# Kernel tuning notes

Hardware: AMD Instinct MI355X
Metric: run time of the kernel (lower is better)

The kernel has to match this reference:

```python
import jax, jax.numpy as jnp
import numpy as np

NEG = -100.0
M2M, M2I, M2D, I2M, I2I, D2M, D2D = range(7)
LOG_Q = float(np.log(0.25))


def _d_chain(fM, aM2D, aD2D):
    """Sequential delete-state recurrence along motif axis k.
    fD[k] = logaddexp(aM2D[k-1] + fM[k-1], aD2D[k-1] + fD[k-1]), fD[0] = NEG.
    fM: (B, K+1); aM2D, aD2D: (B, K+1). Returns (B, K+1)."""
    B, Kp1 = fM.shape
    K = Kp1 - 1

    def step(fd_prev, inp):
        am, ad, fm = inp  # each (B,)
        fd = jnp.logaddexp(am + fm, ad + fd_prev)
        return fd, fd

    init = jnp.full((B,), NEG, dtype=fM.dtype)
    _, fds = jax.lax.scan(step, init, (aM2D[:, :K].T, aD2D[:, :K].T, fM[:, :K].T))
    return jnp.concatenate([init[:, None], fds.T], axis=1)


def _profile_hmm_loss(a, e, x):
    """pHMM forward algorithm (log-space). a: (B,K+1,7), e: (B,K,4), x: (B,L) int.
    Returns -log P(x) per batch element, shape (B,)."""
    B, Kp1, _ = a.shape
    K = Kp1 - 1

    fM0 = jnp.full((B, Kp1), NEG, dtype=a.dtype).at[:, 0].set(0.0)
    fI0 = jnp.full((B, Kp1), NEG, dtype=a.dtype)
    fD0 = _d_chain(fM0, a[:, :, M2D], a[:, :, D2D])

    def l_step(carry, x_l):
        fM, fI, fD = carry
        # emission for symbol x_l at each match state k: (B, K)
        esel = jnp.take_along_axis(e, x_l[:, None, None].astype(jnp.int32), axis=2)[:, :, 0]
        prev = jnp.logaddexp(
            jnp.logaddexp(a[:, :K, M2M] + fM[:, :K], a[:, :K, I2M] + fI[:, :K]),
            a[:, :K, D2M] + fD[:, :K],
        )
        fM_new = jnp.concatenate([jnp.full((B, 1), NEG, dtype=a.dtype), esel + prev], axis=1)
        fI_new = LOG_Q + jnp.logaddexp(a[:, :, M2I] + fM, a[:, :, I2I] + fI)
        fD_new = _d_chain(fM_new, a[:, :, M2D], a[:, :, D2D])
        return (fM_new, fI_new, fD_new), None

    (fM, fI, fD), _ = jax.lax.scan(l_step, (fM0, fI0, fD0), x.T)

    final = jnp.stack(
        [fM[:, K] + a[:, K, M2M], fI[:, K] + a[:, K, I2M], fD[:, K] + a[:, K, D2M]],
        axis=1,
    )
    return -jax.nn.logsumexp(final, axis=1)


def _kld_loss(mus, logvars):
    return -0.5 * jnp.sum(1.0 + logvars - mus * mus - jnp.exp(logvars), axis=1)


def setup_inputs() -> dict:
    key = jax.random.key(0)
    k1, k2, k3, k4, k5 = jax.random.split(key, 5)
    B, K, L, E = 4096, 64, 128, 16
    batch_input = jax.random.randint(k1, (B, L), 0, 4, dtype=jnp.int32)
    transition_probs = jax.random.normal(k2, (B, K + 1, 7), dtype=jnp.float32)
    emission_probs = jax.random.normal(k3, (B, K, 4), dtype=jnp.float32)
    mus = jax.random.normal(k4, (B, E), dtype=jnp.float32)
    logvars = jax.random.normal(k5, (B, E), dtype=jnp.float32)
    return {
        "batch_input": batch_input,
        "transition_probs": transition_probs,
        "emission_probs": emission_probs,
        "mus": mus,
        "logvars": logvars,
    }


def reference(batch_input, transition_probs, emission_probs, mus, logvars):
    beta = 1.0
    recon = jnp.mean(_profile_hmm_loss(transition_probs, emission_probs, batch_input))
    kld = jnp.mean(_kld_loss(mus, logvars))
    return recon + beta * kld
```

## Files before the change

### kernel.cpp

```cpp
#include <hip/hip_runtime.h>
#include <math.h>


namespace {

constexpr float kLog2e = 1.4426950408889634f;
constexpr float kLn2   = 0.6931471805599453f;

__device__ __forceinline__ float fexp(float x) {
    return __builtin_amdgcn_exp2f(x * kLog2e);
}

__device__ __forceinline__ float rflf(float x) {
    return __builtin_bit_cast(float,
        __builtin_amdgcn_readfirstlane(__builtin_bit_cast(int, x)));
}

template <int CTRL, bool BC>
__device__ __forceinline__ float dppf(float old, float src) {
    int r = __builtin_amdgcn_update_dpp(__builtin_bit_cast(int, old),
                                        __builtin_bit_cast(int, src),
                                        CTRL, 0xF, 0xF, BC);
    return __builtin_bit_cast(float, r);
}

__global__ __launch_bounds__(256) void phmm_vae_kernel(
    const int* __restrict__ xg,
    const float* __restrict__ ag,
    const float* __restrict__ eg,
    const float* __restrict__ mug,
    const float* __restrict__ lvg,
    float* __restrict__ out, int B)
{
    const int tid  = threadIdx.x;
    const int lane = tid & 63;
    const int wv   = tid >> 6;
    const int b    = (blockIdx.x << 2) + wv;

    __shared__ float part[4];
    float contrib = 0.0f;

    if (b < B) {
        const float* ab = ag + (size_t)b * 455;
        const float* eb = eg + (size_t)b * 256;
        const int*   xb = xg + (size_t)b * 128;

        const int j = lane;
        const float a2 = ab[j * 7 + 2];
        const float a6 = ab[j * 7 + 6];
        const float a5 = ab[(j + 1) * 7 + 5];
        const float A1M2M  = fexp(ab[(j + 1) * 7 + 0]);
        const float QA1M2I = 0.25f * fexp(ab[(j + 1) * 7 + 1]);
        const float A1I2M  = fexp(ab[(j + 1) * 7 + 3]);
        const float QA1I2I = 0.25f * fexp(ab[(j + 1) * 7 + 4]);
        const float A0M2M = fexp(ab[0]);
        const float D0f = rflf(0.25f * fexp(ab[4]));
        const float G0f = rflf(0.25f * fexp(ab[3] + ab[1] - ab[0]));

        float4 ev = *reinterpret_cast<const float4*>(eb + j * 4);
        const float E0 = fexp(ev.x), E1 = fexp(ev.y);
        const float E2 = fexp(ev.z), E3 = fexp(ev.w);

        const int xlo = xb[lane];
        const int xhi = xb[64 + lane];
        const unsigned long long b0lo = __ballot(xlo & 1);
        const unsigned long long b1lo = __ballot(xlo & 2);
        const unsigned long long b0hi = __ballot(xhi & 1);
        const unsigned long long b1hi = __ballot(xhi & 2);

        const float a5p = dppf<0x138, false>(0.0f, a5);
        const float dh  = fexp(a6 + a5 - a5p);
        const float wM2D = fexp(a2 + a5);
        const float Cf0 = wM2D * dppf<0x138, false>(0.0f, E0);
        const float Cf1 = wM2D * dppf<0x138, false>(0.0f, E1);
        const float Cf2 = wM2D * dppf<0x138, false>(0.0f, E2);
        const float Cf3 = wM2D * dppf<0x138, false>(0.0f, E3);

        auto bfr = [](float x) -> unsigned {
            unsigned u = __builtin_bit_cast(unsigned, x);
            return (u + 0x8000u) >> 16;
        };
        const int E10 = (int)((bfr(E1) << 16) | bfr(E0));
        const int E32 = (int)((bfr(E3) << 16) | bfr(E2));
        const int C10 = (int)((bfr(Cf1) << 16) | bfr(Cf0));
        const int C32 = (int)((bfr(Cf3) << 16) | bfr(Cf2));

        const float V1 = dh;
        const float V2 = V1 * dppf<0x111, false>(1.0f, V1);
        const float V4 = V2 * dppf<0x112, false>(1.0f, V2);
        const float V8 = V4 * dppf<0x114, false>(1.0f, V4);
        const float V1m = (lane >= 1)  ? V1 : 0.0f;
        const float V2m = (lane >= 2)  ? V2 : 0.0f;
        const float V4m = (lane >= 4)  ? V4 : 0.0f;
        const float V8m = (lane >= 8)  ? V8 : 0.0f;
        float Q = dh;
        Q *= dppf<0x111, false>(1.0f, Q);
        Q *= dppf<0x112, false>(1.0f, Q);
        Q *= dppf<0x114, false>(1.0f, Q);
        Q *= dppf<0x118, false>(1.0f, Q);
        const int   row = lane >> 4;
        const float Q47 = __shfl(Q, 47, 64);
        const float QmA = (row == 1 || row == 3) ? Q : 0.0f;
        const float QmB = (row == 2) ? Q : ((row == 3) ? Q * Q47 : 0.0f);

        float y0 = (lane == 0) ? wM2D : 0.0f;
        y0 = fmaf(V1m, dppf<0x111, true>(0.0f, y0), y0);
        y0 = fmaf(V2m, dppf<0x112, true>(0.0f, y0), y0);
        y0 = fmaf(V4m, dppf<0x114, true>(0.0f, y0), y0);
        y0 = fmaf(V8m, dppf<0x118, true>(0.0f, y0), y0);
        y0 = fmaf(QmA, dppf<0x142, true>(0.0f, y0), y0);
        y0 = fmaf(QmB, dppf<0x143, true>(0.0f, y0), y0);

        auto sel_of = [&](int l) -> int {
            const unsigned long long m0 = (l & 64) ? b0hi : b0lo;
            const unsigned long long m1 = (l & 64) ? b1hi : b1lo;
            const int sh = l & 63;
            unsigned s = (unsigned)((m0 >> sh) & 1ull) |
                         ((unsigned)((m1 >> sh) & 1ull) << 1);
            return (int)(0x00000C0Cu + s * 0x02020000u + 0x01000000u);
        };

        float fM = 0.0f, fI = 0.0f;
        float pl = y0;
        float p0 = A0M2M;
        float LS = 0.0f;

        const int sel0 = sel_of(0);
        float E = __builtin_bit_cast(float,
            __builtin_amdgcn_perm((unsigned)E32, (unsigned)E10, (unsigned)sel0));
        float C = __builtin_bit_cast(float,
            __builtin_amdgcn_perm((unsigned)C32, (unsigned)C10, (unsigned)sel0));

#pragma unroll 8
        for (int l = 0; l < 128; ++l) {
            const int seln = sel_of((l + 1) & 127);
            const float mul_s = (l == 0) ? G0f : D0f;

            float y, pv, En, Cn;
            asm("v_mul_f32 %[fI], %[QI2I], %[fI]\n\t"
                "v_mov_b32 %[pv], %[p0]\n\t"
                "v_perm_b32 %[En], %[e32], %[e10], %[sel]\n\t"
                "v_perm_b32 %[Cn], %[c32], %[c10], %[sel]\n\t"
                "v_mov_b32_dpp %[pv], %[pl] wave_shr:1 row_mask:0xf bank_mask:0xf\n\t"
                "v_fmac_f32 %[fI], %[QM2I], %[fM]\n\t"
                "v_mul_f32 %[p0], %[mul], %[p0]\n\t"
                "v_mul_f32_dpp %[y], %[pv], %[C] wave_shr:1 row_mask:0xf bank_mask:0xf bound_ctrl:0\n\t"
                "v_mul_f32 %[fM], %[E], %[pv]\n\t"
                "s_nop 0\n\t"
                "v_fmac_f32_dpp %[y], %[y], %[V1] row_shr:1 row_mask:0xf bank_mask:0xf bound_ctrl:0\n\t"
                "s_nop 1\n\t"
                "v_fmac_f32_dpp %[y], %[y], %[V2] row_shr:2 row_mask:0xf bank_mask:0xf bound_ctrl:0\n\t"
                "s_nop 1\n\t"
                "v_fmac_f32_dpp %[y], %[y], %[V4] row_shr:4 row_mask:0xf bank_mask:0xf bound_ctrl:0\n\t"
                "s_nop 1\n\t"
                "v_fmac_f32_dpp %[y], %[y], %[V8] row_shr:8 row_mask:0xf bank_mask:0xf bound_ctrl:0\n\t"
                "s_nop 1\n\t"
                "v_fmac_f32_dpp %[y], %[y], %[QmA] row_bcast:15 row_mask:0xf bank_mask:0xf bound_ctrl:0\n\t"
                "s_nop 1\n\t"
                "v_fmac_f32_dpp %[y], %[y], %[QmB] row_bcast:31 row_mask:0xf bank_mask:0xf bound_ctrl:0\n\t"
                "v_fmac_f32 %[y], %[I2M], %[fI]\n\t"
                "v_fmac_f32 %[y], %[M2M], %[fM]"
                : [y] "=&v"(y), [pv] "=&v"(pv), [En] "=&v"(En), [Cn] "=&v"(Cn),
                  [fM] "+v"(fM), [fI] "+v"(fI), [p0] "+v"(p0)
                : [pl] "v"(pl), [E] "v"(E), [C] "v"(C),
                  [e32] "v"(E32), [e10] "v"(E10),
                  [c32] "v"(C32), [c10] "v"(C10),
                  [V1] "v"(V1m), [V2] "v"(V2m), [V4] "v"(V4m), [V8] "v"(V8m),
                  [QmA] "v"(QmA), [QmB] "v"(QmB),
                  [QI2I] "v"(QA1I2I), [QM2I] "v"(QA1M2I),
                  [I2M] "v"(A1I2M), [M2M] "v"(A1M2M),
                  [sel] "s"(seln), [mul] "s"(mul_s));
            pl = y;
            E = En;
            C = Cn;

            if ((l & 15) == 15) {
                float m = fmaxf(fmaxf(fM, fI), pl);
                m = fmaxf(m, dppf<0xB1,  true>(0.0f, m));
                m = fmaxf(m, dppf<0x4E,  true>(0.0f, m));
                m = fmaxf(m, dppf<0x141, true>(0.0f, m));
                m = fmaxf(m, dppf<0x140, true>(0.0f, m));
                m = fmaxf(m, 1e-35f);
                int mb = __builtin_bit_cast(int, m);
                unsigned u0 = (unsigned)__builtin_amdgcn_readlane(mb, 0);
                unsigned u1 = (unsigned)__builtin_amdgcn_readlane(mb, 16);
                unsigned u2 = (unsigned)__builtin_amdgcn_readlane(mb, 32);
                unsigned u3 = (unsigned)__builtin_amdgcn_readlane(mb, 48);
                unsigned ua = u0 > u1 ? u0 : u1;
                unsigned ub = u2 > u3 ? u2 : u3;
                unsigned um = ua > ub ? ua : ub;
                int ee = (int)(um >> 23);
                float r = __builtin_bit_cast(float, (unsigned)(254 - ee) << 23);
                LS += (float)(ee - 127);
                fM *= r; fI *= r; pl *= r; p0 *= r;
            }
        }

        const float Fv = __shfl(pl, 63, 64);
        const float loss = -(__builtin_amdgcn_logf(Fv) + LS) * kLn2;

        float kt = 0.0f;
        if (lane < 16) {
            float mu = mug[(size_t)b * 16 + lane];
            float lv = lvg[(size_t)b * 16 + lane];
            kt = 1.0f + lv - mu * mu - fexp(lv);
        }
        kt += __shfl_xor(kt, 1, 64);
        kt += __shfl_xor(kt, 2, 64);
        kt += __shfl_xor(kt, 4, 64);
        kt += __shfl_xor(kt, 8, 64);
        float kldb = __shfl(-0.5f * kt, 0, 64);

        contrib = (loss + kldb) * (1.0f / 4096.0f);
    }

    if (lane == 63) part[wv] = (b < B) ? contrib : 0.0f;
    __syncthreads();
    if (tid == 0) {
        atomicAdd(out, part[0] + part[1] + part[2] + part[3]);
    }
}

}

extern "C" void kernel_launch(void* const* d_in, const int* in_sizes, int n_in,
                              void* d_out, int out_size, void* d_ws, size_t ws_size,
                              hipStream_t stream) {
    const int*   x  = (const int*)d_in[0];
    const float* a  = (const float*)d_in[1];
    const float* e  = (const float*)d_in[2];
    const float* mu = (const float*)d_in[3];
    const float* lv = (const float*)d_in[4];
    float* out = (float*)d_out;

    const int B = in_sizes[0] / 128;
    const int grid = (B + 3) / 4;

    phmm_vae_kernel<<<grid, 256, 0, stream>>>(x, a, e, mu, lv, out, B);
}
```

Before: 91.26 us.

## Replace DPP row-scan with ds_bpermute Hillis-Steele scan in delete chain

Replaces the in-loop delete-state prefix scan, which used row-level DPP shifts plus row_bcast fixups, with six ds_bpermute_b32 steps using full-wave lane offsets and precomputed prefix-product weights. It also unrolls the main loop further and simplifies the periodic rescaling to a full DPP max reduction read from lane 63, accumulating the scale exponent as an integer. The bpermute path goes through the LDS crossbar and waits on lgkmcnt at every step, so each step on the critical serial chain likely has much higher latency than a DPP op.

```diff
diff --git a/kernel.cpp b/kernel.cpp
--- a/kernel.cpp
+++ b/kernel.cpp
@@ -85,31 +85,34 @@
         const int C10 = (int)((bfr(Cf1) << 16) | bfr(Cf0));
         const int C32 = (int)((bfr(Cf3) << 16) | bfr(Cf2));
 
-        const float V1 = dh;
-        const float V2 = V1 * dppf<0x111, false>(1.0f, V1);
-        const float V4 = V2 * dppf<0x112, false>(1.0f, V2);
-        const float V8 = V4 * dppf<0x114, false>(1.0f, V4);
-        const float V1m = (lane >= 1)  ? V1 : 0.0f;
-        const float V2m = (lane >= 2)  ? V2 : 0.0f;
-        const float V4m = (lane >= 4)  ? V4 : 0.0f;
-        const float V8m = (lane >= 8)  ? V8 : 0.0f;
-        float Q = dh;
-        Q *= dppf<0x111, false>(1.0f, Q);
-        Q *= dppf<0x112, false>(1.0f, Q);
-        Q *= dppf<0x114, false>(1.0f, Q);
-        Q *= dppf<0x118, false>(1.0f, Q);
-        const int   row = lane >> 4;
-        const float Q47 = __shfl(Q, 47, 64);
-        const float QmA = (row == 1 || row == 3) ? Q : 0.0f;
-        const float QmB = (row == 2) ? Q : ((row == 3) ? Q * Q47 : 0.0f);
+        float t;
+        const float W1 = dh;
+        t = __shfl_up(W1, 1, 64);  const float W2  = (lane >= 1)  ? W1 * t : W1;
+        t = __shfl_up(W2, 2, 64);  const float W4  = (lane >= 2)  ? W2 * t : W2;
+        t = __shfl_up(W4, 4, 64);  const float W8  = (lane >= 4)  ? W4 * t : W4;
+        t = __shfl_up(W8, 8, 64);  const float W16 = (lane >= 8)  ? W8 * t : W8;
+        t = __shfl_up(W16, 16, 64); const float W32 = (lane >= 16) ? W16 * t : W16;
+        const float W1m  = (lane >= 1)  ? W1  : 0.0f;
+        const float W2m  = (lane >= 2)  ? W2  : 0.0f;
+        const float W4m  = (lane >= 4)  ? W4  : 0.0f;
+        const float W8m  = (lane >= 8)  ? W8  : 0.0f;
+        const float W16m = (lane >= 16) ? W16 : 0.0f;
+        const float W32m = (lane >= 32) ? W32 : 0.0f;
+
+        const int a1  = ((lane - 1)  & 63) << 2;
+        const int a2i = ((lane - 2)  & 63) << 2;
+        const int a4  = ((lane - 4)  & 63) << 2;
+        const int a8  = ((lane - 8)  & 63) << 2;
+        const int a16 = ((lane - 16) & 63) << 2;
+        const int a32 = ((lane - 32) & 63) << 2;
 
         float y0 = (lane == 0) ? wM2D : 0.0f;
-        y0 = fmaf(V1m, dppf<0x111, true>(0.0f, y0), y0);
-        y0 = fmaf(V2m, dppf<0x112, true>(0.0f, y0), y0);
-        y0 = fmaf(V4m, dppf<0x114, true>(0.0f, y0), y0);
-        y0 = fmaf(V8m, dppf<0x118, true>(0.0f, y0), y0);
-        y0 = fmaf(QmA, dppf<0x142, true>(0.0f, y0), y0);
-        y0 = fmaf(QmB, dppf<0x143, true>(0.0f, y0), y0);
+        t = __shfl_up(y0, 1, 64);  y0 = fmaf(W1m,  t, y0);
+        t = __shfl_up(y0, 2, 64);  y0 = fmaf(W2m,  t, y0);
+        t = __shfl_up(y0, 4, 64);  y0 = fmaf(W4m,  t, y0);
+        t = __shfl_up(y0, 8, 64);  y0 = fmaf(W8m,  t, y0);
+        t = __shfl_up(y0, 16, 64); y0 = fmaf(W16m, t, y0);
+        t = __shfl_up(y0, 32, 64); y0 = fmaf(W32m, t, y0);
 
         auto sel_of = [&](int l) -> int {
             const unsigned long long m0 = (l & 64) ? b0hi : b0lo;
@@ -123,7 +126,7 @@
         float fM = 0.0f, fI = 0.0f;
         float pl = y0;
         float p0 = A0M2M;
-        float LS = 0.0f;
+        int   lsI = 0;
 
         const int sel0 = sel_of(0);
         float E = __builtin_bit_cast(float,
@@ -131,12 +134,12 @@
         float C = __builtin_bit_cast(float,
             __builtin_amdgcn_perm((unsigned)C32, (unsigned)C10, (unsigned)sel0));
 
-#pragma unroll 8
+#pragma unroll 16
         for (int l = 0; l < 128; ++l) {
             const int seln = sel_of((l + 1) & 127);
             const float mul_s = (l == 0) ? G0f : D0f;
 
-            float y, pv, En, Cn;
+            float y, pv, tt, En, Cn;
             asm("v_mul_f32 %[fI], %[QI2I], %[fI]\n\t"
                 "v_mov_b32 %[pv], %[p0]\n\t"
                 "v_perm_b32 %[En], %[e32], %[e10], %[sel]\n\t"
@@ -146,27 +149,36 @@
                 "v_mul_f32 %[p0], %[mul], %[p0]\n\t"
                 "v_mul_f32_dpp %[y], %[pv], %[C] wave_shr:1 row_mask:0xf bank_mask:0xf bound_ctrl:0\n\t"
                 "v_mul_f32 %[fM], %[E], %[pv]\n\t"
-                "s_nop 0\n\t"
-                "v_fmac_f32_dpp %[y], %[y], %[V1] row_shr:1 row_mask:0xf bank_mask:0xf bound_ctrl:0\n\t"
-                "s_nop 1\n\t"
-                "v_fmac_f32_dpp %[y], %[y], %[V2] row_shr:2 row_mask:0xf bank_mask:0xf bound_ctrl:0\n\t"
-                "s_nop 1\n\t"
-                "v_fmac_f32_dpp %[y], %[y], %[V4] row_shr:4 row_mask:0xf bank_mask:0xf bound_ctrl:0\n\t"
-                "s_nop 1\n\t"
-                "v_fmac_f32_dpp %[y], %[y], %[V8] row_shr:8 row_mask:0xf bank_mask:0xf bound_ctrl:0\n\t"
-                "s_nop 1\n\t"
-                "v_fmac_f32_dpp %[y], %[y], %[QmA] row_bcast:15 row_mask:0xf bank_mask:0xf bound_ctrl:0\n\t"
-                "s_nop 1\n\t"
-                "v_fmac_f32_dpp %[y], %[y], %[QmB] row_bcast:31 row_mask:0xf bank_mask:0xf bound_ctrl:0\n\t"
+                "ds_bpermute_b32 %[tt], %[a1], %[y]\n\t"
+                "s_waitcnt lgkmcnt(0)\n\t"
+                "v_fmac_f32 %[y], %[W1], %[tt]\n\t"
+                "ds_bpermute_b32 %[tt], %[a2], %[y]\n\t"
+                "s_waitcnt lgkmcnt(0)\n\t"
+                "v_fmac_f32 %[y], %[W2], %[tt]\n\t"
+                "ds_bpermute_b32 %[tt], %[a4], %[y]\n\t"
+                "s_waitcnt lgkmcnt(0)\n\t"
+                "v_fmac_f32 %[y], %[W4], %[tt]\n\t"
+                "ds_bpermute_b32 %[tt], %[a8], %[y]\n\t"
+                "s_waitcnt lgkmcnt(0)\n\t"
+                "v_fmac_f32 %[y], %[W8], %[tt]\n\t"
+                "ds_bpermute_b32 %[tt], %[a16], %[y]\n\t"
+                "s_waitcnt lgkmcnt(0)\n\t"
+                "v_fmac_f32 %[y], %[W16], %[tt]\n\t"
+                "ds_bpermute_b32 %[tt], %[a32], %[y]\n\t"
+                "s_waitcnt lgkmcnt(0)\n\t"
+                "v_fmac_f32 %[y], %[W32], %[tt]\n\t"
                 "v_fmac_f32 %[y], %[I2M], %[fI]\n\t"
                 "v_fmac_f32 %[y], %[M2M], %[fM]"
-                : [y] "=&v"(y), [pv] "=&v"(pv), [En] "=&v"(En), [Cn] "=&v"(Cn),
+                : [y] "=&v"(y), [pv] "=&v"(pv), [tt] "=&v"(tt),
+                  [En] "=&v"(En), [Cn] "=&v"(Cn),
                   [fM] "+v"(fM), [fI] "+v"(fI), [p0] "+v"(p0)
                 : [pl] "v"(pl), [E] "v"(E), [C] "v"(C),
                   [e32] "v"(E32), [e10] "v"(E10),
                   [c32] "v"(C32), [c10] "v"(C10),
-                  [V1] "v"(V1m), [V2] "v"(V2m), [V4] "v"(V4m), [V8] "v"(V8m),
-                  [QmA] "v"(QmA), [QmB] "v"(QmB),
+                  [W1] "v"(W1m), [W2] "v"(W2m), [W4] "v"(W4m),
+                  [W8] "v"(W8m), [W16] "v"(W16m), [W32] "v"(W32m),
+                  [a1] "v"(a1), [a2] "v"(a2i), [a4] "v"(a4),
+                  [a8] "v"(a8), [a16] "v"(a16), [a32] "v"(a32),
                   [QI2I] "v"(QA1I2I), [QM2I] "v"(QA1M2I),
                   [I2M] "v"(A1I2M), [M2M] "v"(A1M2M),
                   [sel] "s"(seln), [mul] "s"(mul_s));
@@ -180,24 +192,19 @@
                 m = fmaxf(m, dppf<0x4E,  true>(0.0f, m));
                 m = fmaxf(m, dppf<0x141, true>(0.0f, m));
                 m = fmaxf(m, dppf<0x140, true>(0.0f, m));
+                m = fmaxf(m, dppf<0x142, true>(0.0f, m));
+                m = fmaxf(m, dppf<0x143, true>(0.0f, m));
                 m = fmaxf(m, 1e-35f);
-                int mb = __builtin_bit_cast(int, m);
-                unsigned u0 = (unsigned)__builtin_amdgcn_readlane(mb, 0);
-                unsigned u1 = (unsigned)__builtin_amdgcn_readlane(mb, 16);
-                unsigned u2 = (unsigned)__builtin_amdgcn_readlane(mb, 32);
-                unsigned u3 = (unsigned)__builtin_amdgcn_readlane(mb, 48);
-                unsigned ua = u0 > u1 ? u0 : u1;
-                unsigned ub = u2 > u3 ? u2 : u3;
-                unsigned um = ua > ub ? ua : ub;
-                int ee = (int)(um >> 23);
+                int ee = __builtin_amdgcn_readlane(
+                             __builtin_bit_cast(int, m), 63) >> 23;
                 float r = __builtin_bit_cast(float, (unsigned)(254 - ee) << 23);
-                LS += (float)(ee - 127);
+                lsI += ee - 127;
                 fM *= r; fI *= r; pl *= r; p0 *= r;
             }
         }
 
         const float Fv = __shfl(pl, 63, 64);
-        const float loss = -(__builtin_amdgcn_logf(Fv) + LS) * kLn2;
+        const float loss = -(__builtin_amdgcn_logf(Fv) + (float)lsI) * kLn2;
 
         float kt = 0.0f;
         if (lane < 16) {
```

Result: slower. 113.5 us (+24.4%).
